# Kernel tuning notes

Hardware: AMD Instinct MI355X
Metric: run time of the kernel (lower is better)

## Reference

```python
import jax, jax.numpy as jnp
import numpy as np

NUM_HEADS = 8  # from init_kwargs
SR = 2         # sr_ratio from init_kwargs


def layernorm(t, g, b, eps=1e-5):
    mu = jnp.mean(t, axis=-1, keepdims=True)
    var = jnp.mean((t - mu) ** 2, axis=-1, keepdims=True)
    return (t - mu) * jax.lax.rsqrt(var + eps) * g + b


def setup_inputs() -> dict:
    key = jax.random.key(0)
    ks = jax.random.split(key, 6)
    B, C = 4, 256
    Hx = Wx = 64
    Hz = Wz = 32
    N = Hz * Wz + Hx * Wx  # 5120 (template tokens first, then search tokens)
    s = 0.02
    return {
        "x": jax.random.normal(ks[0], (B, N, C), jnp.float32),
        "Wq": jax.random.normal(ks[1], (C, C), jnp.float32) * s,          # nn.Linear(dim, dim, bias=False)
        "Wkv": jax.random.normal(ks[2], (2 * C, C), jnp.float32) * s,     # nn.Linear(dim, 2*dim, bias=False)
        "Wsr": jax.random.normal(ks[3], (C, C, SR, SR), jnp.float32) * s, # Conv2d(dim, dim, k=sr, stride=sr) OIHW
        "bsr": jnp.zeros((C,), jnp.float32),
        "gamma": jnp.ones((C,), jnp.float32),
        "beta": jnp.zeros((C,), jnp.float32),
        "Wproj": jax.random.normal(ks[4], (C, C), jnp.float32) * s,
        "bproj": jnp.zeros((C,), jnp.float32),
        "H_x": Hx, "W_x": Wx, "H_z": Hz, "W_z": Wz,
    }


def reference(x, Wq, Wkv, Wsr, bsr, gamma, beta, Wproj, bproj, H_x, W_x, H_z, W_z):
    B, N, C = x.shape
    h = NUM_HEADS
    d = C // h
    scale = d ** -0.5
    Nz, Nx = H_z * W_z, H_x * W_x

    # q for all tokens: [B, h, N, d]
    q = (x @ Wq.T).reshape(B, N, h, d).transpose(0, 2, 1, 3)

    # spatial reduction (sr_ratio > 1 branch): strided conv + layernorm on each stream
    z_tok, x_tok = x[:, :Nz], x[:, Nz:]
    ker = jnp.transpose(Wsr, (2, 3, 1, 0))  # OIHW -> HWIO

    def sr_branch(t, H, W):
        img = t.reshape(B, H, W, C)  # NHWC; same layout as torch NCHW reshape
        out = jax.lax.conv_general_dilated(
            img, ker, window_strides=(SR, SR), padding="VALID",
            dimension_numbers=("NHWC", "HWIO", "NHWC")) + bsr
        out = out.reshape(B, -1, C)
        return layernorm(out, gamma, beta)

    x_ = sr_branch(x_tok, H_x, W_x)  # [B, (Hx/sr)*(Wx/sr), C]
    z_ = sr_branch(z_tok, H_z, W_z)  # [B, (Hz/sr)*(Wz/sr), C]
    zL = z_.shape[1]
    cat = jnp.concatenate([z_, x_], axis=1)  # [B, L, C]

    kv = (cat @ Wkv.T).reshape(B, -1, 2, h, d).transpose(2, 0, 3, 1, 4)  # [2, B, h, L, d]
    k, v = kv[0], kv[1]

    q_z, q_x = q[:, :, :Nz], q[:, :, Nz:]
    k_z, v_z = k[:, :, :zL], v[:, :, :zL]

    # template queries attend only to reduced template keys/values
    attn_z = jax.nn.softmax(jnp.einsum("bhqd,bhkd->bhqk", q_z, k_z) * scale, axis=-1)
    out_z = jnp.einsum("bhqk,bhkd->bhqd", attn_z, v_z).transpose(0, 2, 1, 3).reshape(B, Nz, C)

    # search queries attend to full (template+search) reduced keys/values
    attn_x = jax.nn.softmax(jnp.einsum("bhqd,bhkd->bhqk", q_x, k) * scale, axis=-1)
    out_x = jnp.einsum("bhqk,bhkd->bhqd", attn_x, v).transpose(0, 2, 1, 3).reshape(B, Nx, C)

    out = jnp.concatenate([out_z, out_x], axis=1)
    return out @ Wproj.T + bproj
```

## Files before the change

### kernel.cpp

```cpp
#include <hip/hip_runtime.h>
#include <hip/hip_bf16.h>
#include <cstddef>

#define BATCH 4
#define CCH 256
#define NHEAD 8
#define DHEAD 32
#define NZ 1024
#define NX 4096
#define NTOK 5120
#define LKV 1280
#define QC 0.25503486f

typedef __attribute__((ext_vector_type(8))) short bf16x8;
typedef __attribute__((ext_vector_type(4))) float floatx4;

__device__ inline short f2bf(float f) {
  __hip_bfloat16 h = __float2bfloat16(f);
  return __builtin_bit_cast(short, h);
}
__device__ inline unsigned int pk2(float a, float b) {
  unsigned int lo = (unsigned short)f2bf(a);
  unsigned int hi = (unsigned short)f2bf(b);
  return lo | (hi << 16);
}
__device__ inline unsigned int pk2f(float a, float b) {
  unsigned int ua = __builtin_bit_cast(unsigned int, a) + 0x8000u;
  unsigned int ub = __builtin_bit_cast(unsigned int, b) + 0x8000u;
  return __builtin_amdgcn_perm(ub, ua, 0x07060302u);
}

__global__ __launch_bounds__(256) void cvt_bf16(const float* __restrict__ src,
                                                short* __restrict__ dst, int n8) {
  int i = blockIdx.x * 256 + threadIdx.x;
  if (i >= n8) return;
  float4 v0 = ((const float4*)src)[i * 2];
  float4 v1 = ((const float4*)src)[i * 2 + 1];
  uint4 u;
  u.x = pk2(v0.x, v0.y); u.y = pk2(v0.z, v0.w);
  u.z = pk2(v1.x, v1.y); u.w = pk2(v1.z, v1.w);
  ((uint4*)dst)[i] = u;
}

__global__ __launch_bounds__(256) void reorder_wsr(const float* __restrict__ Wsr,
                                                   short* __restrict__ Wkb) {
  int i = blockIdx.x * 256 + threadIdx.x;
  int co = i >> 10;
  int rem = i & 1023;
  int di = rem >> 9, dj = (rem >> 8) & 1, ci = rem & 255;
  Wkb[i] = f2bf(Wsr[((co * 256 + ci) * 2 + di) * 2 + dj]);
}

__global__ __launch_bounds__(256) void im2col_kernel(const short* __restrict__ xbf,
                                                     short* __restrict__ patch) {
  int blk = blockIdx.x;
  int b = blk / 1280, t = blk % 1280;
  int c = threadIdx.x;
#pragma unroll
  for (int di = 0; di < 2; ++di)
#pragma unroll
    for (int dj = 0; dj < 2; ++dj) {
      int src;
      if (t < 256) {
        int oi = t >> 4, oj = t & 15;
        src = b * NTOK + (2 * oi + di) * 32 + (2 * oj + dj);
      } else {
        int tt = t - 256;
        int oi = tt >> 5, oj = tt & 31;
        src = b * NTOK + NZ + (2 * oi + di) * 64 + (2 * oj + dj);
      }
      patch[(size_t)blk * 1024 + di * 512 + dj * 256 + c] = xbf[(size_t)src * CCH + c];
    }
}

#define MG_PROLOG()                                                          \
  __shared__ short As[64][72];                                               \
  __shared__ short Bs[64][72];                                               \
  int bm = blockIdx.y * 64, bn = blockIdx.x * 64;                            \
  int tid = threadIdx.x;                                                     \
  int wave = tid >> 6, lane = tid & 63, lg = lane >> 4, lr = lane & 15;      \
  int sr = tid >> 2, sc = tid & 3;                                           \
  floatx4 acc[4] = {{0.f,0.f,0.f,0.f},{0.f,0.f,0.f,0.f},                     \
                    {0.f,0.f,0.f,0.f},{0.f,0.f,0.f,0.f}};                    \
  (void)lane;

#define MG_LOOP(Abf, Bbf, K)                                                 \
  for (int k0 = 0; k0 < (K); k0 += 64) {                                     \
    bf16x8 a0 = *(const bf16x8*)&(Abf)[(size_t)(bm + sr) * (K) + k0 + sc * 8];       \
    bf16x8 a1 = *(const bf16x8*)&(Abf)[(size_t)(bm + sr) * (K) + k0 + (sc + 4) * 8]; \
    bf16x8 b0 = *(const bf16x8*)&(Bbf)[(size_t)(bn + sr) * (K) + k0 + sc * 8];       \
    bf16x8 b1 = *(const bf16x8*)&(Bbf)[(size_t)(bn + sr) * (K) + k0 + (sc + 4) * 8]; \
    __syncthreads();                                                         \
    *(bf16x8*)&As[sr][sc * 8] = a0;                                          \
    *(bf16x8*)&As[sr][(sc + 4) * 8] = a1;                                    \
    *(bf16x8*)&Bs[sr][sc * 8] = b0;                                          \
    *(bf16x8*)&Bs[sr][(sc + 4) * 8] = b1;                                    \
    __syncthreads();                                                         \
    bf16x8 af0 = *(bf16x8*)&As[wave * 16 + lr][lg * 8];                      \
    bf16x8 af1 = *(bf16x8*)&As[wave * 16 + lr][32 + lg * 8];                 \
    _Pragma("unroll") for (int n = 0; n < 4; ++n) {                          \
      bf16x8 bf0 = *(bf16x8*)&Bs[n * 16 + lr][lg * 8];                       \
      bf16x8 bf1 = *(bf16x8*)&Bs[n * 16 + lr][32 + lg * 8];                  \
      acc[n] = __builtin_amdgcn_mfma_f32_16x16x32_bf16(af0, bf0, acc[n], 0, 0, 0); \
      acc[n] = __builtin_amdgcn_mfma_f32_16x16x32_bf16(af1, bf1, acc[n], 0, 0, 0); \
    }                                                                        \
  }

__global__ __launch_bounds__(256) void gemm_q(const short* __restrict__ A,
                                              const short* __restrict__ Bm,
                                              short* __restrict__ qbf) {
  MG_PROLOG()
  MG_LOOP(A, Bm, 256)
#pragma unroll
  for (int n = 0; n < 4; ++n) {
    int c = bn + 16 * n + lr;
    int h = c >> 5, d = c & 31;
#pragma unroll
    for (int reg = 0; reg < 4; ++reg) {
      int m = bm + wave * 16 + 4 * lg + reg;
      int b = m / NTOK, tok = m - b * NTOK;
      qbf[((size_t)(b * 8 + h) * NTOK + tok) * 32 + d] = f2bf(acc[n][reg] * QC);
    }
  }
}

__global__ __launch_bounds__(256) void gemm_conv(const short* __restrict__ A,
                                                 const short* __restrict__ Bm,
                                                 float* __restrict__ Cm) {
  MG_PROLOG()
  MG_LOOP(A, Bm, 1024)
#pragma unroll
  for (int n = 0; n < 4; ++n) {
    int c = bn + 16 * n + lr;
#pragma unroll
    for (int reg = 0; reg < 4; ++reg) {
      int m = bm + wave * 16 + 4 * lg + reg;
      Cm[(size_t)m * 256 + c] = acc[n][reg];
    }
  }
}

__global__ __launch_bounds__(256) void gemm_kv(const short* __restrict__ A,
                                               const short* __restrict__ Bm,
                                               short* __restrict__ Kbf,
                                               short* __restrict__ Vtb) {
  MG_PROLOG()
  MG_LOOP(A, Bm, 256)
#pragma unroll
  for (int n = 0; n < 4; ++n) {
    int c = bn + 16 * n + lr;
#pragma unroll
    for (int reg = 0; reg < 4; ++reg) {
      int m = bm + wave * 16 + 4 * lg + reg;
      int b = m / LKV, kvg = m - b * LKV;
      if (c < 256) {
        int h = c >> 5, d = c & 31;
        Kbf[((size_t)(b * 8 + h) * LKV + kvg) * 32 + d] = f2bf(acc[n][reg]);
      } else {
        int cc = c - 256;
        int h = cc >> 5, d = cc & 31;
        int tile = kvg >> 6, kvin = kvg & 63;
        Vtb[(((size_t)(b * 8 + h) * 20 + tile) * 32 + d) * 64 + kvin] = f2bf(acc[n][reg]);
      }
    }
  }
}

__global__ __launch_bounds__(256) void gemm_proj(const short* __restrict__ A,
                                                 const short* __restrict__ Bm,
                                                 const float* __restrict__ bias,
                                                 float* __restrict__ Cm) {
  MG_PROLOG()
  MG_LOOP(A, Bm, 256)
#pragma unroll
  for (int n = 0; n < 4; ++n) {
    int c = bn + 16 * n + lr;
    float bv = bias[c];
#pragma unroll
    for (int reg = 0; reg < 4; ++reg) {
      int m = bm + wave * 16 + 4 * lg + reg;
      Cm[(size_t)m * 256 + c] = acc[n][reg] + bv;
    }
  }
}

__global__ __launch_bounds__(256) void ln_kernel(const float* __restrict__ cat_pre,
                                                 const float* __restrict__ bsr,
                                                 const float* __restrict__ gamma,
                                                 const float* __restrict__ beta,
                                                 short* __restrict__ catb) {
  int row = blockIdx.x * 4 + (threadIdx.x >> 6);
  int lane = threadIdx.x & 63;
  float4 v = *(const float4*)&cat_pre[(size_t)row * 256 + lane * 4];
  float4 bb = *(const float4*)&bsr[lane * 4];
  v.x += bb.x; v.y += bb.y; v.z += bb.z; v.w += bb.w;
  float s = (v.x + v.y) + (v.z + v.w);
#pragma unroll
  for (int mask = 1; mask < 64; mask <<= 1) s += __shfl_xor(s, mask, 64);
  float mu = s * (1.f / 256.f);
  float4 dv;
  dv.x = v.x - mu; dv.y = v.y - mu; dv.z = v.z - mu; dv.w = v.w - mu;
  float q = dv.x * dv.x + dv.y * dv.y + dv.z * dv.z + dv.w * dv.w;
#pragma unroll
  for (int mask = 1; mask < 64; mask <<= 1) q += __shfl_xor(q, mask, 64);
  float rs = rsqrtf(q * (1.f / 256.f) + 1e-5f);
  float4 g = *(const float4*)&gamma[lane * 4];
  float4 be = *(const float4*)&beta[lane * 4];
  uint2 st;
  st.x = pk2(dv.x * rs * g.x + be.x, dv.y * rs * g.y + be.y);
  st.y = pk2(dv.z * rs * g.z + be.z, dv.w * rs * g.w + be.w);
  *(uint2*)&catb[(size_t)row * 256 + lane * 4] = st;
}

__global__ __launch_bounds__(256) void attn_fused(const short* __restrict__ qbf,
                                                  const short* __restrict__ Kbf,
                                                  const short* __restrict__ Vtb,
                                                  short* __restrict__ attn_out) {
  int blk = blockIdx.x;
  int bh, q0, kvlen;
  if (blk < 1024) {
    bh = blk >> 5; q0 = NZ + (blk & 31) * 128; kvlen = LKV;
  } else {
    int idx = blk - 1024;
    bh = idx >> 3; q0 = (idx & 7) * 128; kvlen = 256;
  }
  int b = bh >> 3, hh = bh & 7;
  int tid = threadIdx.x;
  int wave = tid >> 6, lane = tid & 63, lg = lane >> 4, lr = lane & 15;

  __shared__ short Ps[4][32][72];

  int qtok = q0 + wave * 32;
  const short* qb = qbf + ((size_t)bh * NTOK + qtok) * 32;
  bf16x8 qf[2];
#pragma unroll
  for (int qi = 0; qi < 2; ++qi)
    qf[qi] = *(const bf16x8*)&qb[(16 * qi + lr) * 32 + lg * 8];

  const short* Kb = Kbf + (size_t)bh * LKV * 32;
  const short* Vb = Vtb + (size_t)bh * 20 * 2048;

  floatx4 oacc[2][2];
#pragma unroll
  for (int qi = 0; qi < 2; ++qi)
#pragma unroll
    for (int n = 0; n < 2; ++n) oacc[qi][n] = (floatx4){0.f, 0.f, 0.f, 0.f};
  float lsum[2] = {0.f, 0.f};

  bf16x8 kfc[4], vfc[2][2];
#pragma unroll
  for (int m = 0; m < 4; ++m)
    kfc[m] = *(const bf16x8*)&Kb[(size_t)(16 * m + lr) * 32 + lg * 8];
#pragma unroll
  for (int n = 0; n < 2; ++n)
#pragma unroll
    for (int kb = 0; kb < 2; ++kb)
      vfc[n][kb] = *(const bf16x8*)&Vb[(16 * n + lr) * 64 + kb * 32 + lg * 8];

  for (int l0 = 0; l0 < kvlen; l0 += 64) {
#pragma unroll
    for (int qi = 0; qi < 2; ++qi) {
      floatx4 st[4];
#pragma unroll
      for (int m = 0; m < 4; ++m)
        st[m] = __builtin_amdgcn_mfma_f32_16x16x32_bf16(
            kfc[m], qf[qi], (floatx4){0.f, 0.f, 0.f, 0.f}, 0, 0, 0);
      int pr = 16 * qi + lr;
#pragma unroll
      for (int m = 0; m < 4; ++m) {
        float p0 = __builtin_amdgcn_exp2f(st[m][0]);
        float p1 = __builtin_amdgcn_exp2f(st[m][1]);
        float p2 = __builtin_amdgcn_exp2f(st[m][2]);
        float p3 = __builtin_amdgcn_exp2f(st[m][3]);
        lsum[qi] += (p0 + p1) + (p2 + p3);
        *(unsigned int*)&Ps[wave][pr][16 * m + 4 * lg]     = pk2f(p0, p1);
        *(unsigned int*)&Ps[wave][pr][16 * m + 4 * lg + 2] = pk2f(p2, p3);
      }
    }

    bf16x8 kfn[4], vfn[2][2];
    int l1 = l0 + 64;
    if (l1 < kvlen) {
      const short* Vbt = Vb + (l1 >> 6) * 2048;
#pragma unroll
      for (int m = 0; m < 4; ++m)
        kfn[m] = *(const bf16x8*)&Kb[(size_t)(l1 + 16 * m + lr) * 32 + lg * 8];
#pragma unroll
      for (int n = 0; n < 2; ++n)
#pragma unroll
        for (int kb = 0; kb < 2; ++kb)
          vfn[n][kb] = *(const bf16x8*)&Vbt[(16 * n + lr) * 64 + kb * 32 + lg * 8];
    }

#pragma unroll
    for (int qi = 0; qi < 2; ++qi)
#pragma unroll
      for (int kb = 0; kb < 2; ++kb) {
        bf16x8 pf = *(bf16x8*)&Ps[wave][16 * qi + lr][kb * 32 + lg * 8];
#pragma unroll
        for (int n = 0; n < 2; ++n)
          oacc[qi][n] = __builtin_amdgcn_mfma_f32_16x16x32_bf16(pf, vfc[n][kb], oacc[qi][n], 0, 0, 0);
      }

#pragma unroll
    for (int m = 0; m < 4; ++m) kfc[m] = kfn[m];
#pragma unroll
    for (int n = 0; n < 2; ++n)
#pragma unroll
      for (int kb = 0; kb < 2; ++kb) vfc[n][kb] = vfn[n][kb];
  }

#pragma unroll
  for (int qi = 0; qi < 2; ++qi) {
    lsum[qi] += __shfl_xor(lsum[qi], 16, 64);
    lsum[qi] += __shfl_xor(lsum[qi], 32, 64);
  }

#pragma unroll
  for (int qi = 0; qi < 2; ++qi)
#pragma unroll
    for (int reg = 0; reg < 4; ++reg) {
      float lv = __shfl(lsum[qi], 4 * lg + reg, 64);
      float inv = 1.f / lv;
      int gr = b * NTOK + qtok + 16 * qi + 4 * lg + reg;
      short* ob = attn_out + (size_t)gr * CCH + hh * DHEAD;
      ob[lr]      = f2bf(oacc[qi][0][reg] * inv);
      ob[16 + lr] = f2bf(oacc[qi][1][reg] * inv);
    }
}

extern "C" void kernel_launch(void* const* d_in, const int* in_sizes, int n_in,
                              void* d_out, int out_size, void* d_ws, size_t ws_size,
                              hipStream_t stream) {
  (void)in_sizes; (void)n_in; (void)out_size; (void)ws_size;
  const float* x     = (const float*)d_in[0];
  const float* Wq    = (const float*)d_in[1];
  const float* Wkv   = (const float*)d_in[2];
  const float* Wsr   = (const float*)d_in[3];
  const float* bsr   = (const float*)d_in[4];
  const float* gamma = (const float*)d_in[5];
  const float* beta  = (const float*)d_in[6];
  const float* Wproj = (const float*)d_in[7];
  const float* bproj = (const float*)d_in[8];
  float* out = (float*)d_out;
  float* ws  = (float*)d_ws;

  short* qbf      = (short*)ws;
  short* attn_out = (short*)(ws + 2621440);
  short* patch    = (short*)(ws + 5242880);
  short* xbf      = (short*)(ws + 7864320);
  float* cat_pre  = ws + 10485760;
  short* catb     = (short*)(ws + 11796480);
  short* Kbf      = (short*)(ws + 12451840);
  short* Vtb      = (short*)(ws + 13107200);
  short* Wqb      = (short*)(ws + 13762560);
  short* Wkvb     = (short*)(ws + 13795328);
  short* Wkb      = (short*)(ws + 13860864);
  short* Wprojb   = (short*)(ws + 13991936);

  cvt_bf16<<<2560, 256, 0, stream>>>(x, xbf, 655360);
  cvt_bf16<<<32, 256, 0, stream>>>(Wq, Wqb, 8192);
  cvt_bf16<<<64, 256, 0, stream>>>(Wkv, Wkvb, 16384);
  cvt_bf16<<<32, 256, 0, stream>>>(Wproj, Wprojb, 8192);
  reorder_wsr<<<1024, 256, 0, stream>>>(Wsr, Wkb);
  im2col_kernel<<<BATCH * LKV, 256, 0, stream>>>(xbf, patch);
  gemm_q<<<dim3(4, 320), 256, 0, stream>>>(xbf, Wqb, qbf);
  gemm_conv<<<dim3(4, 80), 256, 0, stream>>>(patch, Wkb, cat_pre);
  ln_kernel<<<1280, 256, 0, stream>>>(cat_pre, bsr, gamma, beta, catb);
  gemm_kv<<<dim3(8, 80), 256, 0, stream>>>(catb, Wkvb, Kbf, Vtb);
  attn_fused<<<1280, 256, 0, stream>>>(qbf, Kbf, Vtb, attn_out);
  gemm_proj<<<dim3(4, 320), 256, 0, stream>>>(attn_out, Wprojb, bproj, out);
}
```

Measured before the change: 217.1 us.

## Fuse x bf16 conversion into GEMM/im2col, enlarge GEMM tiles, widen attention per-wave rows

Drops the separate fp32-to-bf16 conversion of x: im2col and the Q GEMM now read fp32 x directly and convert inline. The Q, KV and projection GEMMs move from 64x64 tiles with 256 threads to 128x128 tiles with 512 threads, giving more reuse per shared-memory load. The attention kernel drops to 2 waves per block, each handling 64 query rows, so every loaded K/V fragment is reused across more queries. This raises register pressure, and the larger tiles leave fewer blocks for the kv GEMM (160).

```diff
diff --git a/kernel.cpp b/kernel.cpp
--- a/kernel.cpp
+++ b/kernel.cpp
@@ -51,7 +51,7 @@
   Wkb[i] = f2bf(Wsr[((co * 256 + ci) * 2 + di) * 2 + dj]);
 }
 
-__global__ __launch_bounds__(256) void im2col_kernel(const short* __restrict__ xbf,
+__global__ __launch_bounds__(256) void im2col_kernel(const float* __restrict__ x,
                                                      short* __restrict__ patch) {
   int blk = blockIdx.x;
   int b = blk / 1280, t = blk % 1280;
@@ -69,66 +69,174 @@
         int oi = tt >> 5, oj = tt & 31;
         src = b * NTOK + NZ + (2 * oi + di) * 64 + (2 * oj + dj);
       }
-      patch[(size_t)blk * 1024 + di * 512 + dj * 256 + c] = xbf[(size_t)src * CCH + c];
-    }
-}
-
-#define MG_PROLOG()                                                          \
-  __shared__ short As[64][72];                                               \
-  __shared__ short Bs[64][72];                                               \
-  int bm = blockIdx.y * 64, bn = blockIdx.x * 64;                            \
+      patch[(size_t)blk * 1024 + di * 512 + dj * 256 + c] = f2bf(x[(size_t)src * CCH + c]);
+    }
+}
+
+#define G128_PROLOG()                                                        \
+  __shared__ short As[128][72];                                              \
+  __shared__ short Bs[128][72];                                              \
+  int bm = blockIdx.y * 128, bn = blockIdx.x * 128;                          \
   int tid = threadIdx.x;                                                     \
   int wave = tid >> 6, lane = tid & 63, lg = lane >> 4, lr = lane & 15;      \
+  int wm = wave >> 2, wn = wave & 3;                                         \
   int sr = tid >> 2, sc = tid & 3;                                           \
-  floatx4 acc[4] = {{0.f,0.f,0.f,0.f},{0.f,0.f,0.f,0.f},                     \
-                    {0.f,0.f,0.f,0.f},{0.f,0.f,0.f,0.f}};                    \
-  (void)lane;
-
-#define MG_LOOP(Abf, Bbf, K)                                                 \
+  floatx4 acc[4][2];                                                         \
+  _Pragma("unroll") for (int mi = 0; mi < 4; ++mi)                           \
+      _Pragma("unroll") for (int ni = 0; ni < 2; ++ni)                       \
+          acc[mi][ni] = (floatx4){0.f, 0.f, 0.f, 0.f};
+
+#define G128_MFMA_BODY()                                                     \
+    __syncthreads();                                                         \
+    bf16x8 af0[4], af1[4], bf0[2], bf1[2];                                   \
+    _Pragma("unroll") for (int mi = 0; mi < 4; ++mi) {                       \
+      af0[mi] = *(bf16x8*)&As[wm * 64 + mi * 16 + lr][lg * 8];               \
+      af1[mi] = *(bf16x8*)&As[wm * 64 + mi * 16 + lr][32 + lg * 8];          \
+    }                                                                        \
+    _Pragma("unroll") for (int ni = 0; ni < 2; ++ni) {                       \
+      bf0[ni] = *(bf16x8*)&Bs[wn * 32 + ni * 16 + lr][lg * 8];               \
+      bf1[ni] = *(bf16x8*)&Bs[wn * 32 + ni * 16 + lr][32 + lg * 8];          \
+    }                                                                        \
+    _Pragma("unroll") for (int mi = 0; mi < 4; ++mi)                         \
+      _Pragma("unroll") for (int ni = 0; ni < 2; ++ni) {                     \
+        acc[mi][ni] = __builtin_amdgcn_mfma_f32_16x16x32_bf16(af0[mi], bf0[ni], acc[mi][ni], 0, 0, 0); \
+        acc[mi][ni] = __builtin_amdgcn_mfma_f32_16x16x32_bf16(af1[mi], bf1[ni], acc[mi][ni], 0, 0, 0); \
+      }
+
+#define G128_LOOP_BF16(Abf, Bbf, K)                                          \
   for (int k0 = 0; k0 < (K); k0 += 64) {                                     \
-    bf16x8 a0 = *(const bf16x8*)&(Abf)[(size_t)(bm + sr) * (K) + k0 + sc * 8];       \
-    bf16x8 a1 = *(const bf16x8*)&(Abf)[(size_t)(bm + sr) * (K) + k0 + (sc + 4) * 8]; \
-    bf16x8 b0 = *(const bf16x8*)&(Bbf)[(size_t)(bn + sr) * (K) + k0 + sc * 8];       \
-    bf16x8 b1 = *(const bf16x8*)&(Bbf)[(size_t)(bn + sr) * (K) + k0 + (sc + 4) * 8]; \
+    bf16x8 a0 = *(const bf16x8*)&(Abf)[(size_t)(bm + sr) * (K) + k0 + sc * 16];     \
+    bf16x8 a1 = *(const bf16x8*)&(Abf)[(size_t)(bm + sr) * (K) + k0 + sc * 16 + 8]; \
+    bf16x8 b0 = *(const bf16x8*)&(Bbf)[(size_t)(bn + sr) * (K) + k0 + sc * 16];     \
+    bf16x8 b1 = *(const bf16x8*)&(Bbf)[(size_t)(bn + sr) * (K) + k0 + sc * 16 + 8]; \
     __syncthreads();                                                         \
-    *(bf16x8*)&As[sr][sc * 8] = a0;                                          \
-    *(bf16x8*)&As[sr][(sc + 4) * 8] = a1;                                    \
-    *(bf16x8*)&Bs[sr][sc * 8] = b0;                                          \
-    *(bf16x8*)&Bs[sr][(sc + 4) * 8] = b1;                                    \
+    *(bf16x8*)&As[sr][sc * 16] = a0;                                         \
+    *(bf16x8*)&As[sr][sc * 16 + 8] = a1;                                     \
+    *(bf16x8*)&Bs[sr][sc * 16] = b0;                                         \
+    *(bf16x8*)&Bs[sr][sc * 16 + 8] = b1;                                     \
+    G128_MFMA_BODY()                                                         \
+  }
+
+#define G128_LOOP_F32A(Af, Bbf, K)                                           \
+  for (int k0 = 0; k0 < (K); k0 += 64) {                                     \
+    const float4* ap = (const float4*)&(Af)[(size_t)(bm + sr) * (K) + k0 + sc * 16]; \
+    float4 f0 = ap[0], f1 = ap[1], f2 = ap[2], f3 = ap[3];                   \
+    uint4 ua, ub;                                                            \
+    ua.x = pk2(f0.x, f0.y); ua.y = pk2(f0.z, f0.w);                          \
+    ua.z = pk2(f1.x, f1.y); ua.w = pk2(f1.z, f1.w);                          \
+    ub.x = pk2(f2.x, f2.y); ub.y = pk2(f2.z, f2.w);                          \
+    ub.z = pk2(f3.x, f3.y); ub.w = pk2(f3.z, f3.w);                          \
+    bf16x8 b0 = *(const bf16x8*)&(Bbf)[(size_t)(bn + sr) * (K) + k0 + sc * 16];     \
+    bf16x8 b1 = *(const bf16x8*)&(Bbf)[(size_t)(bn + sr) * (K) + k0 + sc * 16 + 8]; \
     __syncthreads();                                                         \
-    bf16x8 af0 = *(bf16x8*)&As[wave * 16 + lr][lg * 8];                      \
-    bf16x8 af1 = *(bf16x8*)&As[wave * 16 + lr][32 + lg * 8];                 \
-    _Pragma("unroll") for (int n = 0; n < 4; ++n) {                          \
-      bf16x8 bf0 = *(bf16x8*)&Bs[n * 16 + lr][lg * 8];                       \
-      bf16x8 bf1 = *(bf16x8*)&Bs[n * 16 + lr][32 + lg * 8];                  \
-      acc[n] = __builtin_amdgcn_mfma_f32_16x16x32_bf16(af0, bf0, acc[n], 0, 0, 0); \
-      acc[n] = __builtin_amdgcn_mfma_f32_16x16x32_bf16(af1, bf1, acc[n], 0, 0, 0); \
-    }                                                                        \
-  }
-
-__global__ __launch_bounds__(256) void gemm_q(const short* __restrict__ A,
-                                              const short* __restrict__ Bm,
-                                              short* __restrict__ qbf) {
-  MG_PROLOG()
-  MG_LOOP(A, Bm, 256)
-#pragma unroll
-  for (int n = 0; n < 4; ++n) {
-    int c = bn + 16 * n + lr;
+    *(uint4*)&As[sr][sc * 16] = ua;                                          \
+    *(uint4*)&As[sr][sc * 16 + 8] = ub;                                      \
+    *(bf16x8*)&Bs[sr][sc * 16] = b0;                                         \
+    *(bf16x8*)&Bs[sr][sc * 16 + 8] = b1;                                     \
+    G128_MFMA_BODY()                                                         \
+  }
+
+__global__ __launch_bounds__(512) void gemm_q128(const float* __restrict__ A,
+                                                 const short* __restrict__ Bm,
+                                                 short* __restrict__ qbf) {
+  G128_PROLOG()
+  G128_LOOP_F32A(A, Bm, 256)
+#pragma unroll
+  for (int ni = 0; ni < 2; ++ni) {
+    int c = bn + wn * 32 + ni * 16 + lr;
     int h = c >> 5, d = c & 31;
 #pragma unroll
-    for (int reg = 0; reg < 4; ++reg) {
-      int m = bm + wave * 16 + 4 * lg + reg;
-      int b = m / NTOK, tok = m - b * NTOK;
-      qbf[((size_t)(b * 8 + h) * NTOK + tok) * 32 + d] = f2bf(acc[n][reg] * QC);
-    }
+    for (int mi = 0; mi < 4; ++mi)
+#pragma unroll
+      for (int reg = 0; reg < 4; ++reg) {
+        int m = bm + wm * 64 + mi * 16 + 4 * lg + reg;
+        int b = m / NTOK, tok = m - b * NTOK;
+        qbf[((size_t)(b * 8 + h) * NTOK + tok) * 32 + d] = f2bf(acc[mi][ni][reg] * QC);
+      }
+  }
+}
+
+__global__ __launch_bounds__(512) void gemm_kv128(const short* __restrict__ A,
+                                                  const short* __restrict__ Bm,
+                                                  short* __restrict__ Kbf,
+                                                  short* __restrict__ Vtb) {
+  G128_PROLOG()
+  G128_LOOP_BF16(A, Bm, 256)
+#pragma unroll
+  for (int ni = 0; ni < 2; ++ni) {
+    int c = bn + wn * 32 + ni * 16 + lr;
+#pragma unroll
+    for (int mi = 0; mi < 4; ++mi)
+#pragma unroll
+      for (int reg = 0; reg < 4; ++reg) {
+        int m = bm + wm * 64 + mi * 16 + 4 * lg + reg;
+        int b = m / LKV, kvg = m - b * LKV;
+        if (c < 256) {
+          int h = c >> 5, d = c & 31;
+          Kbf[((size_t)(b * 8 + h) * LKV + kvg) * 32 + d] = f2bf(acc[mi][ni][reg]);
+        } else {
+          int cc = c - 256;
+          int h = cc >> 5, d = cc & 31;
+          int tile = kvg >> 6, kvin = kvg & 63;
+          Vtb[(((size_t)(b * 8 + h) * 20 + tile) * 32 + d) * 64 + kvin] = f2bf(acc[mi][ni][reg]);
+        }
+      }
+  }
+}
+
+__global__ __launch_bounds__(512) void gemm_proj128(const short* __restrict__ A,
+                                                    const short* __restrict__ Bm,
+                                                    const float* __restrict__ bias,
+                                                    float* __restrict__ Cm) {
+  G128_PROLOG()
+  G128_LOOP_BF16(A, Bm, 256)
+#pragma unroll
+  for (int ni = 0; ni < 2; ++ni) {
+    int c = bn + wn * 32 + ni * 16 + lr;
+    float bv = bias[c];
+#pragma unroll
+    for (int mi = 0; mi < 4; ++mi)
+#pragma unroll
+      for (int reg = 0; reg < 4; ++reg) {
+        int m = bm + wm * 64 + mi * 16 + 4 * lg + reg;
+        Cm[(size_t)m * 256 + c] = acc[mi][ni][reg] + bv;
+      }
   }
 }
 
 __global__ __launch_bounds__(256) void gemm_conv(const short* __restrict__ A,
                                                  const short* __restrict__ Bm,
                                                  float* __restrict__ Cm) {
-  MG_PROLOG()
-  MG_LOOP(A, Bm, 1024)
+  __shared__ short As[64][72];
+  __shared__ short Bs[64][72];
+  int bm = blockIdx.y * 64, bn = blockIdx.x * 64;
+  int tid = threadIdx.x;
+  int wave = tid >> 6, lane = tid & 63, lg = lane >> 4, lr = lane & 15;
+  int sr = tid >> 2, sc = tid & 3;
+  (void)lane;
+  floatx4 acc[4] = {{0.f,0.f,0.f,0.f},{0.f,0.f,0.f,0.f},
+                    {0.f,0.f,0.f,0.f},{0.f,0.f,0.f,0.f}};
+  for (int k0 = 0; k0 < 1024; k0 += 64) {
+    bf16x8 a0 = *(const bf16x8*)&A[(size_t)(bm + sr) * 1024 + k0 + sc * 8];
+    bf16x8 a1 = *(const bf16x8*)&A[(size_t)(bm + sr) * 1024 + k0 + (sc + 4) * 8];
+    bf16x8 b0 = *(const bf16x8*)&Bm[(size_t)(bn + sr) * 1024 + k0 + sc * 8];
+    bf16x8 b1 = *(const bf16x8*)&Bm[(size_t)(bn + sr) * 1024 + k0 + (sc + 4) * 8];
+    __syncthreads();
+    *(bf16x8*)&As[sr][sc * 8] = a0;
+    *(bf16x8*)&As[sr][(sc + 4) * 8] = a1;
+    *(bf16x8*)&Bs[sr][sc * 8] = b0;
+    *(bf16x8*)&Bs[sr][(sc + 4) * 8] = b1;
+    __syncthreads();
+    bf16x8 af0 = *(bf16x8*)&As[wave * 16 + lr][lg * 8];
+    bf16x8 af1 = *(bf16x8*)&As[wave * 16 + lr][32 + lg * 8];
+#pragma unroll
+    for (int n = 0; n < 4; ++n) {
+      bf16x8 bf0 = *(bf16x8*)&Bs[n * 16 + lr][lg * 8];
+      bf16x8 bf1 = *(bf16x8*)&Bs[n * 16 + lr][32 + lg * 8];
+      acc[n] = __builtin_amdgcn_mfma_f32_16x16x32_bf16(af0, bf0, acc[n], 0, 0, 0);
+      acc[n] = __builtin_amdgcn_mfma_f32_16x16x32_bf16(af1, bf1, acc[n], 0, 0, 0);
+    }
+  }
 #pragma unroll
   for (int n = 0; n < 4; ++n) {
     int c = bn + 16 * n + lr;
@@ -136,50 +244,6 @@
     for (int reg = 0; reg < 4; ++reg) {
       int m = bm + wave * 16 + 4 * lg + reg;
       Cm[(size_t)m * 256 + c] = acc[n][reg];
-    }
-  }
-}
-
-__global__ __launch_bounds__(256) void gemm_kv(const short* __restrict__ A,
-                                               const short* __restrict__ Bm,
-                                               short* __restrict__ Kbf,
-                                               short* __restrict__ Vtb) {
-  MG_PROLOG()
-  MG_LOOP(A, Bm, 256)
-#pragma unroll
-  for (int n = 0; n < 4; ++n) {
-    int c = bn + 16 * n + lr;
-#pragma unroll
-    for (int reg = 0; reg < 4; ++reg) {
-      int m = bm + wave * 16 + 4 * lg + reg;
-      int b = m / LKV, kvg = m - b * LKV;
-      if (c < 256) {
-        int h = c >> 5, d = c & 31;
-        Kbf[((size_t)(b * 8 + h) * LKV + kvg) * 32 + d] = f2bf(acc[n][reg]);
-      } else {
-        int cc = c - 256;
-        int h = cc >> 5, d = cc & 31;
-        int tile = kvg >> 6, kvin = kvg & 63;
-        Vtb[(((size_t)(b * 8 + h) * 20 + tile) * 32 + d) * 64 + kvin] = f2bf(acc[n][reg]);
-      }
-    }
-  }
-}
-
-__global__ __launch_bounds__(256) void gemm_proj(const short* __restrict__ A,
-                                                 const short* __restrict__ Bm,
-                                                 const float* __restrict__ bias,
-                                                 float* __restrict__ Cm) {
-  MG_PROLOG()
-  MG_LOOP(A, Bm, 256)
-#pragma unroll
-  for (int n = 0; n < 4; ++n) {
-    int c = bn + 16 * n + lr;
-    float bv = bias[c];
-#pragma unroll
-    for (int reg = 0; reg < 4; ++reg) {
-      int m = bm + wave * 16 + 4 * lg + reg;
-      Cm[(size_t)m * 256 + c] = acc[n][reg] + bv;
     }
   }
 }
@@ -212,7 +276,7 @@
   *(uint2*)&catb[(size_t)row * 256 + lane * 4] = st;
 }
 
-__global__ __launch_bounds__(256) void attn_fused(const short* __restrict__ qbf,
+__global__ __launch_bounds__(128) void attn_fused(const short* __restrict__ qbf,
                                                   const short* __restrict__ Kbf,
                                                   const short* __restrict__ Vtb,
                                                   short* __restrict__ attn_out) {
@@ -228,24 +292,24 @@
   int tid = threadIdx.x;
   int wave = tid >> 6, lane = tid & 63, lg = lane >> 4, lr = lane & 15;
 
-  __shared__ short Ps[4][32][72];
-
-  int qtok = q0 + wave * 32;
+  __shared__ short Ps[2][64][72];
+
+  int qtok = q0 + wave * 64;
   const short* qb = qbf + ((size_t)bh * NTOK + qtok) * 32;
-  bf16x8 qf[2];
-#pragma unroll
-  for (int qi = 0; qi < 2; ++qi)
+  bf16x8 qf[4];
+#pragma unroll
+  for (int qi = 0; qi < 4; ++qi)
     qf[qi] = *(const bf16x8*)&qb[(16 * qi + lr) * 32 + lg * 8];
 
   const short* Kb = Kbf + (size_t)bh * LKV * 32;
   const short* Vb = Vtb + (size_t)bh * 20 * 2048;
 
-  floatx4 oacc[2][2];
-#pragma unroll
-  for (int qi = 0; qi < 2; ++qi)
+  floatx4 oacc[4][2];
+#pragma unroll
+  for (int qi = 0; qi < 4; ++qi)
 #pragma unroll
     for (int n = 0; n < 2; ++n) oacc[qi][n] = (floatx4){0.f, 0.f, 0.f, 0.f};
-  float lsum[2] = {0.f, 0.f};
+  float lsum[4] = {0.f, 0.f, 0.f, 0.f};
 
   bf16x8 kfc[4], vfc[2][2];
 #pragma unroll
@@ -259,7 +323,7 @@
 
   for (int l0 = 0; l0 < kvlen; l0 += 64) {
 #pragma unroll
-    for (int qi = 0; qi < 2; ++qi) {
+    for (int qi = 0; qi < 4; ++qi) {
       floatx4 st[4];
 #pragma unroll
       for (int m = 0; m < 4; ++m)
@@ -273,8 +337,10 @@
         float p2 = __builtin_amdgcn_exp2f(st[m][2]);
         float p3 = __builtin_amdgcn_exp2f(st[m][3]);
         lsum[qi] += (p0 + p1) + (p2 + p3);
-        *(unsigned int*)&Ps[wave][pr][16 * m + 4 * lg]     = pk2f(p0, p1);
-        *(unsigned int*)&Ps[wave][pr][16 * m + 4 * lg + 2] = pk2f(p2, p3);
+        uint2 w;
+        w.x = pk2f(p0, p1);
+        w.y = pk2f(p2, p3);
+        *(uint2*)&Ps[wave][pr][16 * m + 4 * lg] = w;
       }
     }
 
@@ -293,7 +359,7 @@
     }
 
 #pragma unroll
-    for (int qi = 0; qi < 2; ++qi)
+    for (int qi = 0; qi < 4; ++qi)
 #pragma unroll
       for (int kb = 0; kb < 2; ++kb) {
         bf16x8 pf = *(bf16x8*)&Ps[wave][16 * qi + lr][kb * 32 + lg * 8];
@@ -311,13 +377,13 @@
   }
 
 #pragma unroll
-  for (int qi = 0; qi < 2; ++qi) {
+  for (int qi = 0; qi < 4; ++qi) {
     lsum[qi] += __shfl_xor(lsum[qi], 16, 64);
     lsum[qi] += __shfl_xor(lsum[qi], 32, 64);
   }
 
 #pragma unroll
-  for (int qi = 0; qi < 2; ++qi)
+  for (int qi = 0; qi < 4; ++qi)
 #pragma unroll
     for (int reg = 0; reg < 4; ++reg) {
       float lv = __shfl(lsum[qi], 4 * lg + reg, 64);
@@ -348,26 +414,24 @@
   short* qbf      = (short*)ws;
   short* attn_out = (short*)(ws + 2621440);
   short* patch    = (short*)(ws + 5242880);
-  short* xbf      = (short*)(ws + 7864320);
-  float* cat_pre  = ws + 10485760;
-  short* catb     = (short*)(ws + 11796480);
-  short* Kbf      = (short*)(ws + 12451840);
-  short* Vtb      = (short*)(ws + 13107200);
-  short* Wqb      = (short*)(ws + 13762560);
-  short* Wkvb     = (short*)(ws + 13795328);
-  short* Wkb      = (short*)(ws + 13860864);
-  short* Wprojb   = (short*)(ws + 13991936);
-
-  cvt_bf16<<<2560, 256, 0, stream>>>(x, xbf, 655360);
+  float* cat_pre  = ws + 7864320;
+  short* catb     = (short*)(ws + 9175040);
+  short* Kbf      = (short*)(ws + 9830400);
+  short* Vtb      = (short*)(ws + 10485760);
+  short* Wqb      = (short*)(ws + 11141120);
+  short* Wkvb     = (short*)(ws + 11173888);
+  short* Wkb      = (short*)(ws + 11239424);
+  short* Wprojb   = (short*)(ws + 11370496);
+
   cvt_bf16<<<32, 256, 0, stream>>>(Wq, Wqb, 8192);
   cvt_bf16<<<64, 256, 0, stream>>>(Wkv, Wkvb, 16384);
   cvt_bf16<<<32, 256, 0, stream>>>(Wproj, Wprojb, 8192);
   reorder_wsr<<<1024, 256, 0, stream>>>(Wsr, Wkb);
-  im2col_kernel<<<BATCH * LKV, 256, 0, stream>>>(xbf, patch);
-  gemm_q<<<dim3(4, 320), 256, 0, stream>>>(xbf, Wqb, qbf);
+  im2col_kernel<<<BATCH * LKV, 256, 0, stream>>>(x, patch);
+  gemm_q128<<<dim3(2, 160), 512, 0, stream>>>(x, Wqb, qbf);
   gemm_conv<<<dim3(4, 80), 256, 0, stream>>>(patch, Wkb, cat_pre);
   ln_kernel<<<1280, 256, 0, stream>>>(cat_pre, bsr, gamma, beta, catb);
-  gemm_kv<<<dim3(8, 80), 256, 0, stream>>>(catb, Wkvb, Kbf, Vtb);
-  attn_fused<<<1280, 256, 0, stream>>>(qbf, Kbf, Vtb, attn_out);
-  gemm_proj<<<dim3(4, 320), 256, 0, stream>>>(attn_out, Wprojb, bproj, out);
-}
+  gemm_kv128<<<dim3(4, 40), 512, 0, stream>>>(catb, Wkvb, Kbf, Vtb);
+  attn_fused<<<1280, 128, 0, stream>>>(qbf, Kbf, Vtb, attn_out);
+  gemm_proj128<<<dim3(2, 160), 512, 0, stream>>>(attn_out, Wprojb, bproj, out);
+}
```

Result: faster. 200.0 us (-7.9%).

## Fuse weight prep, drop x bf16 pass, merge Q/conv GEMMs, enlarge attention tiles

Applied to the files above, without the earlier changes.

Merges the four weight conversion and reorder kernels into one launch. The separate bf16 copy of x is removed: im2col and the Q GEMM now read and convert fp32 x directly. The Q and conv GEMMs are combined into one grid so they can run concurrently. Attention now gives each wave 64 query rows instead of 32, halving the block count, and P is stored with wider LDS writes. This cuts launches and a full activation round trip, in exchange for higher register pressure in attention and doubled fp32 reads of x in the Q GEMM.

```diff
diff --git a/kernel.cpp b/kernel.cpp
--- a/kernel.cpp
+++ b/kernel.cpp
@@ -29,11 +29,7 @@
   unsigned int ub = __builtin_bit_cast(unsigned int, b) + 0x8000u;
   return __builtin_amdgcn_perm(ub, ua, 0x07060302u);
 }
-
-__global__ __launch_bounds__(256) void cvt_bf16(const float* __restrict__ src,
-                                                short* __restrict__ dst, int n8) {
-  int i = blockIdx.x * 256 + threadIdx.x;
-  if (i >= n8) return;
+__device__ inline void cvt8(const float* __restrict__ src, short* __restrict__ dst, int i) {
   float4 v0 = ((const float4*)src)[i * 2];
   float4 v1 = ((const float4*)src)[i * 2 + 1];
   uint4 u;
@@ -42,16 +38,31 @@
   ((uint4*)dst)[i] = u;
 }
 
-__global__ __launch_bounds__(256) void reorder_wsr(const float* __restrict__ Wsr,
-                                                   short* __restrict__ Wkb) {
-  int i = blockIdx.x * 256 + threadIdx.x;
-  int co = i >> 10;
-  int rem = i & 1023;
-  int di = rem >> 9, dj = (rem >> 8) & 1, ci = rem & 255;
-  Wkb[i] = f2bf(Wsr[((co * 256 + ci) * 2 + di) * 2 + dj]);
-}
-
-__global__ __launch_bounds__(256) void im2col_kernel(const short* __restrict__ xbf,
+__global__ __launch_bounds__(256) void prep_weights(const float* __restrict__ Wq,
+                                                    const float* __restrict__ Wkv,
+                                                    const float* __restrict__ Wproj,
+                                                    const float* __restrict__ Wsr,
+                                                    short* __restrict__ Wqb,
+                                                    short* __restrict__ Wkvb,
+                                                    short* __restrict__ Wprojb,
+                                                    short* __restrict__ Wkb) {
+  int blk = blockIdx.x, tid = threadIdx.x;
+  if (blk < 32) {
+    cvt8(Wq, Wqb, blk * 256 + tid);
+  } else if (blk < 96) {
+    cvt8(Wkv, Wkvb, (blk - 32) * 256 + tid);
+  } else if (blk < 128) {
+    cvt8(Wproj, Wprojb, (blk - 96) * 256 + tid);
+  } else {
+    int i = (blk - 128) * 256 + tid;
+    int co = i >> 10;
+    int rem = i & 1023;
+    int di = rem >> 9, dj = (rem >> 8) & 1, ci = rem & 255;
+    Wkb[i] = f2bf(Wsr[((co * 256 + ci) * 2 + di) * 2 + dj]);
+  }
+}
+
+__global__ __launch_bounds__(256) void im2col_kernel(const float* __restrict__ x,
                                                      short* __restrict__ patch) {
   int blk = blockIdx.x;
   int b = blk / 1280, t = blk % 1280;
@@ -69,83 +80,115 @@
         int oi = tt >> 5, oj = tt & 31;
         src = b * NTOK + NZ + (2 * oi + di) * 64 + (2 * oj + dj);
       }
-      patch[(size_t)blk * 1024 + di * 512 + dj * 256 + c] = xbf[(size_t)src * CCH + c];
-    }
-}
-
-#define MG_PROLOG()                                                          \
+      patch[(size_t)blk * 1024 + di * 512 + dj * 256 + c] = f2bf(x[(size_t)src * CCH + c]);
+    }
+}
+
+#define G64_DECL()                                                           \
   __shared__ short As[64][72];                                               \
   __shared__ short Bs[64][72];                                               \
-  int bm = blockIdx.y * 64, bn = blockIdx.x * 64;                            \
   int tid = threadIdx.x;                                                     \
-  int wave = tid >> 6, lane = tid & 63, lg = lane >> 4, lr = lane & 15;      \
+  int wave = tid >> 6, lg = (tid & 63) >> 4, lr = tid & 15;                  \
   int sr = tid >> 2, sc = tid & 3;                                           \
   floatx4 acc[4] = {{0.f,0.f,0.f,0.f},{0.f,0.f,0.f,0.f},                     \
-                    {0.f,0.f,0.f,0.f},{0.f,0.f,0.f,0.f}};                    \
-  (void)lane;
-
-#define MG_LOOP(Abf, Bbf, K)                                                 \
-  for (int k0 = 0; k0 < (K); k0 += 64) {                                     \
-    bf16x8 a0 = *(const bf16x8*)&(Abf)[(size_t)(bm + sr) * (K) + k0 + sc * 8];       \
-    bf16x8 a1 = *(const bf16x8*)&(Abf)[(size_t)(bm + sr) * (K) + k0 + (sc + 4) * 8]; \
-    bf16x8 b0 = *(const bf16x8*)&(Bbf)[(size_t)(bn + sr) * (K) + k0 + sc * 8];       \
-    bf16x8 b1 = *(const bf16x8*)&(Bbf)[(size_t)(bn + sr) * (K) + k0 + (sc + 4) * 8]; \
+                    {0.f,0.f,0.f,0.f},{0.f,0.f,0.f,0.f}};
+
+#define G64_MFMA8()                                                          \
     __syncthreads();                                                         \
-    *(bf16x8*)&As[sr][sc * 8] = a0;                                          \
-    *(bf16x8*)&As[sr][(sc + 4) * 8] = a1;                                    \
-    *(bf16x8*)&Bs[sr][sc * 8] = b0;                                          \
-    *(bf16x8*)&Bs[sr][(sc + 4) * 8] = b1;                                    \
-    __syncthreads();                                                         \
-    bf16x8 af0 = *(bf16x8*)&As[wave * 16 + lr][lg * 8];                      \
-    bf16x8 af1 = *(bf16x8*)&As[wave * 16 + lr][32 + lg * 8];                 \
-    _Pragma("unroll") for (int n = 0; n < 4; ++n) {                          \
-      bf16x8 bf0 = *(bf16x8*)&Bs[n * 16 + lr][lg * 8];                       \
-      bf16x8 bf1 = *(bf16x8*)&Bs[n * 16 + lr][32 + lg * 8];                  \
-      acc[n] = __builtin_amdgcn_mfma_f32_16x16x32_bf16(af0, bf0, acc[n], 0, 0, 0); \
-      acc[n] = __builtin_amdgcn_mfma_f32_16x16x32_bf16(af1, bf1, acc[n], 0, 0, 0); \
-    }                                                                        \
-  }
-
-__global__ __launch_bounds__(256) void gemm_q(const short* __restrict__ A,
-                                              const short* __restrict__ Bm,
-                                              short* __restrict__ qbf) {
-  MG_PROLOG()
-  MG_LOOP(A, Bm, 256)
-#pragma unroll
-  for (int n = 0; n < 4; ++n) {
-    int c = bn + 16 * n + lr;
-    int h = c >> 5, d = c & 31;
-#pragma unroll
-    for (int reg = 0; reg < 4; ++reg) {
-      int m = bm + wave * 16 + 4 * lg + reg;
-      int b = m / NTOK, tok = m - b * NTOK;
-      qbf[((size_t)(b * 8 + h) * NTOK + tok) * 32 + d] = f2bf(acc[n][reg] * QC);
-    }
-  }
-}
-
-__global__ __launch_bounds__(256) void gemm_conv(const short* __restrict__ A,
+    {                                                                        \
+      bf16x8 af0 = *(bf16x8*)&As[wave * 16 + lr][lg * 8];                    \
+      bf16x8 af1 = *(bf16x8*)&As[wave * 16 + lr][32 + lg * 8];               \
+      _Pragma("unroll") for (int n = 0; n < 4; ++n) {                        \
+        bf16x8 bf0 = *(bf16x8*)&Bs[n * 16 + lr][lg * 8];                     \
+        bf16x8 bf1 = *(bf16x8*)&Bs[n * 16 + lr][32 + lg * 8];                \
+        acc[n] = __builtin_amdgcn_mfma_f32_16x16x32_bf16(af0, bf0, acc[n], 0, 0, 0); \
+        acc[n] = __builtin_amdgcn_mfma_f32_16x16x32_bf16(af1, bf1, acc[n], 0, 0, 0); \
+      }                                                                      \
+    }
+
+__global__ __launch_bounds__(256) void gemm_qconv(const float* __restrict__ x,
+                                                  const short* __restrict__ Wqb,
+                                                  const short* __restrict__ patch,
+                                                  const short* __restrict__ Wkb,
+                                                  short* __restrict__ qbf,
+                                                  float* __restrict__ cat_pre) {
+  G64_DECL()
+  int bidx = blockIdx.x;
+  if (bidx < 1280) {
+    int bm = (bidx >> 2) * 64, bn = (bidx & 3) * 64;
+    for (int k0 = 0; k0 < 256; k0 += 64) {
+      const float4* ap = (const float4*)&x[(size_t)(bm + sr) * 256 + k0 + sc * 16];
+      float4 f0 = ap[0], f1 = ap[1], f2 = ap[2], f3 = ap[3];
+      uint4 ua, ub;
+      ua.x = pk2(f0.x, f0.y); ua.y = pk2(f0.z, f0.w);
+      ua.z = pk2(f1.x, f1.y); ua.w = pk2(f1.z, f1.w);
+      ub.x = pk2(f2.x, f2.y); ub.y = pk2(f2.z, f2.w);
+      ub.z = pk2(f3.x, f3.y); ub.w = pk2(f3.z, f3.w);
+      bf16x8 b0 = *(const bf16x8*)&Wqb[(size_t)(bn + sr) * 256 + k0 + sc * 8];
+      bf16x8 b1 = *(const bf16x8*)&Wqb[(size_t)(bn + sr) * 256 + k0 + (sc + 4) * 8];
+      __syncthreads();
+      *(uint4*)&As[sr][sc * 16] = ua;
+      *(uint4*)&As[sr][sc * 16 + 8] = ub;
+      *(bf16x8*)&Bs[sr][sc * 8] = b0;
+      *(bf16x8*)&Bs[sr][(sc + 4) * 8] = b1;
+      G64_MFMA8()
+    }
+#pragma unroll
+    for (int n = 0; n < 4; ++n) {
+      int c = bn + 16 * n + lr;
+      int h = c >> 5, d = c & 31;
+#pragma unroll
+      for (int reg = 0; reg < 4; ++reg) {
+        int m = bm + wave * 16 + 4 * lg + reg;
+        int b = m / NTOK, tok = m - b * NTOK;
+        qbf[((size_t)(b * 8 + h) * NTOK + tok) * 32 + d] = f2bf(acc[n][reg] * QC);
+      }
+    }
+  } else {
+    int idx = bidx - 1280;
+    int bm = (idx >> 2) * 64, bn = (idx & 3) * 64;
+    for (int k0 = 0; k0 < 1024; k0 += 64) {
+      bf16x8 a0 = *(const bf16x8*)&patch[(size_t)(bm + sr) * 1024 + k0 + sc * 8];
+      bf16x8 a1 = *(const bf16x8*)&patch[(size_t)(bm + sr) * 1024 + k0 + (sc + 4) * 8];
+      bf16x8 b0 = *(const bf16x8*)&Wkb[(size_t)(bn + sr) * 1024 + k0 + sc * 8];
+      bf16x8 b1 = *(const bf16x8*)&Wkb[(size_t)(bn + sr) * 1024 + k0 + (sc + 4) * 8];
+      __syncthreads();
+      *(bf16x8*)&As[sr][sc * 8] = a0;
+      *(bf16x8*)&As[sr][(sc + 4) * 8] = a1;
+      *(bf16x8*)&Bs[sr][sc * 8] = b0;
+      *(bf16x8*)&Bs[sr][(sc + 4) * 8] = b1;
+      G64_MFMA8()
+    }
+#pragma unroll
+    for (int n = 0; n < 4; ++n) {
+      int c = bn + 16 * n + lr;
+#pragma unroll
+      for (int reg = 0; reg < 4; ++reg) {
+        int m = bm + wave * 16 + 4 * lg + reg;
+        cat_pre[(size_t)m * 256 + c] = acc[n][reg];
+      }
+    }
+  }
+}
+
+__global__ __launch_bounds__(256) void gemm_kv64(const short* __restrict__ A,
                                                  const short* __restrict__ Bm,
-                                                 float* __restrict__ Cm) {
-  MG_PROLOG()
-  MG_LOOP(A, Bm, 1024)
-#pragma unroll
-  for (int n = 0; n < 4; ++n) {
-    int c = bn + 16 * n + lr;
-#pragma unroll
-    for (int reg = 0; reg < 4; ++reg) {
-      int m = bm + wave * 16 + 4 * lg + reg;
-      Cm[(size_t)m * 256 + c] = acc[n][reg];
-    }
-  }
-}
-
-__global__ __launch_bounds__(256) void gemm_kv(const short* __restrict__ A,
-                                               const short* __restrict__ Bm,
-                                               short* __restrict__ Kbf,
-                                               short* __restrict__ Vtb) {
-  MG_PROLOG()
-  MG_LOOP(A, Bm, 256)
+                                                 short* __restrict__ Kbf,
+                                                 short* __restrict__ Vtb) {
+  G64_DECL()
+  int bm = blockIdx.y * 64, bn = blockIdx.x * 64;
+  for (int k0 = 0; k0 < 256; k0 += 64) {
+    bf16x8 a0 = *(const bf16x8*)&A[(size_t)(bm + sr) * 256 + k0 + sc * 8];
+    bf16x8 a1 = *(const bf16x8*)&A[(size_t)(bm + sr) * 256 + k0 + (sc + 4) * 8];
+    bf16x8 b0 = *(const bf16x8*)&Bm[(size_t)(bn + sr) * 256 + k0 + sc * 8];
+    bf16x8 b1 = *(const bf16x8*)&Bm[(size_t)(bn + sr) * 256 + k0 + (sc + 4) * 8];
+    __syncthreads();
+    *(bf16x8*)&As[sr][sc * 8] = a0;
+    *(bf16x8*)&As[sr][(sc + 4) * 8] = a1;
+    *(bf16x8*)&Bs[sr][sc * 8] = b0;
+    *(bf16x8*)&Bs[sr][(sc + 4) * 8] = b1;
+    G64_MFMA8()
+  }
 #pragma unroll
   for (int n = 0; n < 4; ++n) {
     int c = bn + 16 * n + lr;
@@ -166,12 +209,24 @@
   }
 }
 
-__global__ __launch_bounds__(256) void gemm_proj(const short* __restrict__ A,
-                                                 const short* __restrict__ Bm,
-                                                 const float* __restrict__ bias,
-                                                 float* __restrict__ Cm) {
-  MG_PROLOG()
-  MG_LOOP(A, Bm, 256)
+__global__ __launch_bounds__(256) void gemm_proj64(const short* __restrict__ A,
+                                                   const short* __restrict__ Bm,
+                                                   const float* __restrict__ bias,
+                                                   float* __restrict__ Cm) {
+  G64_DECL()
+  int bm = blockIdx.y * 64, bn = blockIdx.x * 64;
+  for (int k0 = 0; k0 < 256; k0 += 64) {
+    bf16x8 a0 = *(const bf16x8*)&A[(size_t)(bm + sr) * 256 + k0 + sc * 8];
+    bf16x8 a1 = *(const bf16x8*)&A[(size_t)(bm + sr) * 256 + k0 + (sc + 4) * 8];
+    bf16x8 b0 = *(const bf16x8*)&Bm[(size_t)(bn + sr) * 256 + k0 + sc * 8];
+    bf16x8 b1 = *(const bf16x8*)&Bm[(size_t)(bn + sr) * 256 + k0 + (sc + 4) * 8];
+    __syncthreads();
+    *(bf16x8*)&As[sr][sc * 8] = a0;
+    *(bf16x8*)&As[sr][(sc + 4) * 8] = a1;
+    *(bf16x8*)&Bs[sr][sc * 8] = b0;
+    *(bf16x8*)&Bs[sr][(sc + 4) * 8] = b1;
+    G64_MFMA8()
+  }
 #pragma unroll
   for (int n = 0; n < 4; ++n) {
     int c = bn + 16 * n + lr;
@@ -218,34 +273,34 @@
                                                   short* __restrict__ attn_out) {
   int blk = blockIdx.x;
   int bh, q0, kvlen;
-  if (blk < 1024) {
-    bh = blk >> 5; q0 = NZ + (blk & 31) * 128; kvlen = LKV;
+  if (blk < 512) {
+    bh = blk >> 4; q0 = NZ + (blk & 15) * 256; kvlen = LKV;
   } else {
-    int idx = blk - 1024;
-    bh = idx >> 3; q0 = (idx & 7) * 128; kvlen = 256;
+    int idx = blk - 512;
+    bh = idx >> 2; q0 = (idx & 3) * 256; kvlen = 256;
   }
   int b = bh >> 3, hh = bh & 7;
   int tid = threadIdx.x;
   int wave = tid >> 6, lane = tid & 63, lg = lane >> 4, lr = lane & 15;
 
-  __shared__ short Ps[4][32][72];
-
-  int qtok = q0 + wave * 32;
+  __shared__ short Ps[4][64][72];
+
+  int qtok = q0 + wave * 64;
   const short* qb = qbf + ((size_t)bh * NTOK + qtok) * 32;
-  bf16x8 qf[2];
-#pragma unroll
-  for (int qi = 0; qi < 2; ++qi)
+  bf16x8 qf[4];
+#pragma unroll
+  for (int qi = 0; qi < 4; ++qi)
     qf[qi] = *(const bf16x8*)&qb[(16 * qi + lr) * 32 + lg * 8];
 
   const short* Kb = Kbf + (size_t)bh * LKV * 32;
   const short* Vb = Vtb + (size_t)bh * 20 * 2048;
 
-  floatx4 oacc[2][2];
-#pragma unroll
-  for (int qi = 0; qi < 2; ++qi)
+  floatx4 oacc[4][2];
+#pragma unroll
+  for (int qi = 0; qi < 4; ++qi)
 #pragma unroll
     for (int n = 0; n < 2; ++n) oacc[qi][n] = (floatx4){0.f, 0.f, 0.f, 0.f};
-  float lsum[2] = {0.f, 0.f};
+  float lsum[4] = {0.f, 0.f, 0.f, 0.f};
 
   bf16x8 kfc[4], vfc[2][2];
 #pragma unroll
@@ -259,7 +314,7 @@
 
   for (int l0 = 0; l0 < kvlen; l0 += 64) {
 #pragma unroll
-    for (int qi = 0; qi < 2; ++qi) {
+    for (int qi = 0; qi < 4; ++qi) {
       floatx4 st[4];
 #pragma unroll
       for (int m = 0; m < 4; ++m)
@@ -273,8 +328,10 @@
         float p2 = __builtin_amdgcn_exp2f(st[m][2]);
         float p3 = __builtin_amdgcn_exp2f(st[m][3]);
         lsum[qi] += (p0 + p1) + (p2 + p3);
-        *(unsigned int*)&Ps[wave][pr][16 * m + 4 * lg]     = pk2f(p0, p1);
-        *(unsigned int*)&Ps[wave][pr][16 * m + 4 * lg + 2] = pk2f(p2, p3);
+        uint2 w;
+        w.x = pk2f(p0, p1);
+        w.y = pk2f(p2, p3);
+        *(uint2*)&Ps[wave][pr][16 * m + 4 * lg] = w;
       }
     }
 
@@ -293,7 +350,7 @@
     }
 
 #pragma unroll
-    for (int qi = 0; qi < 2; ++qi)
+    for (int qi = 0; qi < 4; ++qi)
 #pragma unroll
       for (int kb = 0; kb < 2; ++kb) {
         bf16x8 pf = *(bf16x8*)&Ps[wave][16 * qi + lr][kb * 32 + lg * 8];
@@ -311,13 +368,13 @@
   }
 
 #pragma unroll
-  for (int qi = 0; qi < 2; ++qi) {
+  for (int qi = 0; qi < 4; ++qi) {
     lsum[qi] += __shfl_xor(lsum[qi], 16, 64);
     lsum[qi] += __shfl_xor(lsum[qi], 32, 64);
   }
 
 #pragma unroll
-  for (int qi = 0; qi < 2; ++qi)
+  for (int qi = 0; qi < 4; ++qi)
 #pragma unroll
     for (int reg = 0; reg < 4; ++reg) {
       float lv = __shfl(lsum[qi], 4 * lg + reg, 64);
@@ -348,26 +405,20 @@
   short* qbf      = (short*)ws;
   short* attn_out = (short*)(ws + 2621440);
   short* patch    = (short*)(ws + 5242880);
-  short* xbf      = (short*)(ws + 7864320);
-  float* cat_pre  = ws + 10485760;
-  short* catb     = (short*)(ws + 11796480);
-  short* Kbf      = (short*)(ws + 12451840);
-  short* Vtb      = (short*)(ws + 13107200);
-  short* Wqb      = (short*)(ws + 13762560);
-  short* Wkvb     = (short*)(ws + 13795328);
-  short* Wkb      = (short*)(ws + 13860864);
-  short* Wprojb   = (short*)(ws + 13991936);
-
-  cvt_bf16<<<2560, 256, 0, stream>>>(x, xbf, 655360);
-  cvt_bf16<<<32, 256, 0, stream>>>(Wq, Wqb, 8192);
-  cvt_bf16<<<64, 256, 0, stream>>>(Wkv, Wkvb, 16384);
-  cvt_bf16<<<32, 256, 0, stream>>>(Wproj, Wprojb, 8192);
-  reorder_wsr<<<1024, 256, 0, stream>>>(Wsr, Wkb);
-  im2col_kernel<<<BATCH * LKV, 256, 0, stream>>>(xbf, patch);
-  gemm_q<<<dim3(4, 320), 256, 0, stream>>>(xbf, Wqb, qbf);
-  gemm_conv<<<dim3(4, 80), 256, 0, stream>>>(patch, Wkb, cat_pre);
+  float* cat_pre  = ws + 7864320;
+  short* catb     = (short*)(ws + 9175040);
+  short* Kbf      = (short*)(ws + 9830400);
+  short* Vtb      = (short*)(ws + 10485760);
+  short* Wqb      = (short*)(ws + 11141120);
+  short* Wkvb     = (short*)(ws + 11173888);
+  short* Wkb      = (short*)(ws + 11239424);
+  short* Wprojb   = (short*)(ws + 11370496);
+
+  prep_weights<<<1152, 256, 0, stream>>>(Wq, Wkv, Wproj, Wsr, Wqb, Wkvb, Wprojb, Wkb);
+  im2col_kernel<<<BATCH * LKV, 256, 0, stream>>>(x, patch);
+  gemm_qconv<<<1600, 256, 0, stream>>>(x, Wqb, patch, Wkb, qbf, cat_pre);
   ln_kernel<<<1280, 256, 0, stream>>>(cat_pre, bsr, gamma, beta, catb);
-  gemm_kv<<<dim3(8, 80), 256, 0, stream>>>(catb, Wkvb, Kbf, Vtb);
-  attn_fused<<<1280, 256, 0, stream>>>(qbf, Kbf, Vtb, attn_out);
-  gemm_proj<<<dim3(4, 320), 256, 0, stream>>>(attn_out, Wprojb, bproj, out);
-}
+  gemm_kv64<<<dim3(8, 80), 256, 0, stream>>>(catb, Wkvb, Kbf, Vtb);
+  attn_fused<<<640, 256, 0, stream>>>(qbf, Kbf, Vtb, attn_out);
+  gemm_proj64<<<dim3(4, 320), 256, 0, stream>>>(attn_out, Wprojb, bproj, out);
+}
```

After: 193.2 us. 11.0% less time.
